# Performance work log

Hardware: AMD Instinct MI355X
Metric: run time of the kernel (lower is better)

The kernel has to match this reference:

```python
import jax, jax.numpy as jnp
import numpy as np
from jax import lax

B, C, H, W = 32, 684, 16, 64
HID, A, CK, K = 256, 512, 512, 11


def setup_inputs() -> dict:
    key = jax.random.key(0)
    ks = jax.random.split(key, 12)
    s = 0.02
    return {
        "cnn_features": jax.random.normal(ks[0], (B, C, H, W), jnp.float32),
        "hidden": jax.random.normal(ks[1], (B, HID), jnp.float32),
        "alpha_sum": jax.random.uniform(ks[2], (B, 1, H, W), jnp.float32),
        "image_mask": jnp.ones((B, 1, H, W), jnp.float32),
        # hidden_weight: Linear(HID -> A)
        "Wh": jax.random.normal(ks[3], (A, HID), jnp.float32) * s,
        "bh": jnp.zeros((A,), jnp.float32),
        # encoder_feature_conv: Conv2d(C -> A, 1x1) == pointwise linear
        "Wec": jax.random.normal(ks[4], (A, C), jnp.float32) * s,
        "bec": jnp.zeros((A,), jnp.float32),
        # attention_conv: Conv2d(1 -> CK, 11x11, pad 5, no bias)
        "Wac": jax.random.normal(ks[5], (CK, 1, K, K), jnp.float32) * s,
        # attention_weight: Linear(CK -> A, no bias)
        "Waw": jax.random.normal(ks[6], (A, CK), jnp.float32) * s,
        # alpha_convert: Linear(A -> 1)
        "Wv": jax.random.normal(ks[7], (1, A), jnp.float32) * s,
        "bv": jnp.zeros((1,), jnp.float32),
    }


def reference(cnn_features, hidden, alpha_sum, image_mask,
              Wh, bh, Wec, bec, Wac, Waw, Wv, bv):
    # query = hidden_weight(hidden): [B, A]
    query = hidden @ Wh.T + bh
    # attention_conv(alpha_sum): [B, CK, H, W]
    ast = lax.conv_general_dilated(
        alpha_sum, Wac, window_strides=(1, 1),
        padding=[(K // 2, K // 2), (K // 2, K // 2)],
        dimension_numbers=("NCHW", "OIHW", "NCHW"))
    # attention_weight on permuted conv output: [B, H, W, A]
    coverage_alpha = jnp.einsum("bkhw,ak->bhwa", ast, Waw)
    # encoder_feature_conv (1x1 conv == pointwise linear): [B, H, W, A]
    cnn_trans = jnp.einsum("bchw,ac->bhwa", cnn_features, Wec) + bec
    # additive attention score
    alpha_score = jnp.tanh(query[:, None, None, :] + coverage_alpha + cnn_trans)
    # alpha_convert -> scalar energy per position: [B, H, W]
    energy = jnp.einsum("bhwa,a->bhw", alpha_score, Wv[0]) + bv[0]
    energy = energy - energy.max()  # global max-subtract as in original
    energy_exp = jnp.exp(energy) * image_mask[:, 0]
    denom = energy_exp.sum(axis=(-1, -2))[:, None, None] + 1e-10
    alpha = energy_exp / denom  # [B, H, W]
    alpha_sum_new = alpha[:, None, :, :] + alpha_sum  # [B, 1, H, W]
    # context: weighted spatial sum over features -> [B, C]
    context_vector = jnp.einsum("bhw,bchw->bc", alpha, cnn_features)
    return (context_vector, alpha, alpha_sum_new)
```

## Files before the change

### kernel.cpp

```cpp
#include <hip/hip_runtime.h>
#include <math.h>

#define Bn   32
#define Cn   684
#define Hn   16
#define Wn   64
#define HWn  1024
#define HIDn 256
#define An   512
#define KKn  121
#define CREAL 805
#define CPAD 832
#define NSTEP 26

#define OUT_ALPHA 21888
#define OUT_ASUM  (21888 + 32768)

typedef short short8 __attribute__((ext_vector_type(8)));
typedef float floatx4 __attribute__((ext_vector_type(4)));

__device__ __forceinline__ unsigned short f2bf(float f) {
    union { float f; unsigned int i; } v; v.f = f;
    unsigned int i = v.i;
    return (unsigned short)((i + 0x7fffu + ((i >> 16) & 1u)) >> 16);
}
__device__ __forceinline__ unsigned int pack2bf(float v0, float v1) {
    unsigned int u0 = __float_as_uint(v0), u1 = __float_as_uint(v1);
    u0 = (u0 + 0x7fffu + ((u0 >> 16) & 1u)) >> 16;
    u1 = (u1 + 0x7fffu + ((u1 >> 16) & 1u)) & 0xffff0000u;
    return u0 | u1;
}

__global__ __launch_bounds__(256) void k_prep(
    const float* __restrict__ hidden,
    const float* __restrict__ Wh,
    const float* __restrict__ bh,
    const float* __restrict__ bec,
    const float* __restrict__ Wec,
    const float* __restrict__ Wac,
    const float* __restrict__ Waw,
    float* __restrict__ query,
    unsigned short* __restrict__ VTbf)
{
    __shared__ float sbuf[512];
    const int blk = blockIdx.x, t = threadIdx.x;
    if (blk < 512) {
        const int a = blk;
        sbuf[t]       = Waw[(size_t)a * 512 + t];
        sbuf[t + 256] = Waw[(size_t)a * 512 + t + 256];
        __syncthreads();
        for (int cp = t; cp < Cn; cp += 256)
            VTbf[(size_t)a * CPAD + cp] = f2bf(Wec[(size_t)a * Cn + cp]);
        if (t < KKn) {
            float s = 0.f;
            #pragma unroll 8
            for (int k = 0; k < 512; ++k)
                s = fmaf(sbuf[k], Wac[k * KKn + t], s);
            VTbf[(size_t)a * CPAD + Cn + t] = f2bf(s);
        }
        for (int cp = CREAL + t; cp < CPAD; cp += 256)
            VTbf[(size_t)a * CPAD + cp] = 0;
    } else {
        const int b = blk - 512;
        sbuf[t] = (t < HIDn) ? hidden[b * HIDn + t] : 0.f;
        __syncthreads();
        for (int a = t; a < An; a += 256) {
            const float4* wp = (const float4*)(Wh + (size_t)a * HIDn);
            float s = bh[a] + bec[a];
            #pragma unroll 8
            for (int i = 0; i < HIDn / 4; ++i) {
                float4 w = wp[i];
                s = fmaf(sbuf[4 * i],     w.x, s);
                s = fmaf(sbuf[4 * i + 1], w.y, s);
                s = fmaf(sbuf[4 * i + 2], w.z, s);
                s = fmaf(sbuf[4 * i + 3], w.w, s);
            }
            query[b * An + a] = s;
        }
    }
}

__global__ __launch_bounds__(256, 2) void k_energy(
    const float* __restrict__ X,
    const float* __restrict__ asum,
    const float* __restrict__ Wv,
    const float* __restrict__ query,
    const unsigned short* __restrict__ VTbf,
    float* __restrict__ energy)
{
    __shared__ float plane[11 * 74 + 2];
    __shared__ float qs[512];
    __shared__ float wvs[512];
    __shared__ float red[64 * 65];

    const int t = threadIdx.x;
    const int hh = blockIdx.x, b = blockIdx.y;
    const int w = t >> 6, lane = t & 63;
    const int q = lane >> 4, r = lane & 15;

    for (int i = t; i < 11 * 74; i += 256) {
        int di = i / 74, cc = i - di * 74;
        int h2 = hh + di - 5, w2 = cc - 5;
        float v = 0.f;
        if (h2 >= 0 && h2 < Hn && w2 >= 0 && w2 < Wn)
            v = asum[b * HWn + h2 * Wn + w2];
        plane[i] = v;
    }
    qs[t]        = query[b * An + t];
    qs[t + 256]  = query[b * An + t + 256];
    wvs[t]       = Wv[t];
    wvs[t + 256] = Wv[t + 256];
    __syncthreads();

    floatx4 acc[4][8];
    #pragma unroll
    for (int mf = 0; mf < 4; ++mf)
        #pragma unroll
        for (int nf = 0; nf < 8; ++nf)
            acc[mf][nf] = (floatx4){0.f, 0.f, 0.f, 0.f};

    const float* Xb = X + (size_t)b * Cn * HWn + hh * Wn;
    const unsigned short* Bb = VTbf + (size_t)(w * 128) * CPAD;

    for (int ch = 0; ch < 21; ++ch) {
        const int c0 = ch * 32;
        short8 bfr[8];
        #pragma unroll
        for (int nf = 0; nf < 8; ++nf)
            bfr[nf] = *(const short8*)(Bb + (size_t)(nf * 16 + r) * CPAD + c0 + q * 8);
        short8 af[4];
        #pragma unroll
        for (int mf = 0; mf < 4; ++mf) {
            const int m = mf * 16 + r;
            const float* xp = Xb + (size_t)(c0 + q * 8) * HWn + m;
            unsigned int pk[4];
            #pragma unroll
            for (int jj = 0; jj < 4; ++jj)
                pk[jj] = pack2bf(xp[(size_t)(2 * jj) * HWn], xp[(size_t)(2 * jj + 1) * HWn]);
            union { unsigned int u[4]; short8 s; } cv;
            cv.u[0] = pk[0]; cv.u[1] = pk[1]; cv.u[2] = pk[2]; cv.u[3] = pk[3];
            af[mf] = cv.s;
        }
        #pragma unroll
        for (int mf = 0; mf < 4; ++mf)
            #pragma unroll
            for (int nf = 0; nf < 8; ++nf)
                acc[mf][nf] = __builtin_amdgcn_mfma_f32_16x16x32_bf16(
                    af[mf], bfr[nf], acc[mf][nf], 0, 0, 0);
    }
    for (int ch = 21; ch < NSTEP; ++ch) {
        const int c0 = ch * 32;
        short8 bfr[8];
        #pragma unroll
        for (int nf = 0; nf < 8; ++nf)
            bfr[nf] = *(const short8*)(Bb + (size_t)(nf * 16 + r) * CPAD + c0 + q * 8);
        short8 af[4];
        #pragma unroll
        for (int mf = 0; mf < 4; ++mf) {
            const int m = mf * 16 + r;
            float v[8];
            #pragma unroll
            for (int jj = 0; jj < 8; ++jj) {
                int row = c0 + q * 8 + jj;
                float x;
                if (row < Cn) {
                    x = Xb[(size_t)row * HWn + m];
                } else if (row < CREAL) {
                    int ij = row - Cn; int di = ij / 11, dj = ij - di * 11;
                    x = plane[di * 74 + m + dj];
                } else {
                    x = 0.f;
                }
                v[jj] = x;
            }
            union { unsigned int u[4]; short8 s; } cv;
            #pragma unroll
            for (int jj = 0; jj < 4; ++jj)
                cv.u[jj] = pack2bf(v[2 * jj], v[2 * jj + 1]);
            af[mf] = cv.s;
        }
        #pragma unroll
        for (int mf = 0; mf < 4; ++mf)
            #pragma unroll
            for (int nf = 0; nf < 8; ++nf)
                acc[mf][nf] = __builtin_amdgcn_mfma_f32_16x16x32_bf16(
                    af[mf], bfr[nf], acc[mf][nf], 0, 0, 0);
    }

    float ep[16];
    #pragma unroll
    for (int i = 0; i < 16; ++i) ep[i] = 0.f;
    #pragma unroll
    for (int nf = 0; nf < 8; ++nf) {
        int n = w * 128 + nf * 16 + r;
        float qv = qs[n], wv = wvs[n];
        #pragma unroll
        for (int mf = 0; mf < 4; ++mf)
            #pragma unroll
            for (int rg = 0; rg < 4; ++rg) {
                float x = acc[mf][nf][rg] + qv;
                float e2 = __expf(2.f * x);
                float th = 1.f - 2.f * __builtin_amdgcn_rcpf(e2 + 1.f);
                ep[mf * 4 + rg] += wv * th;
            }
    }
    __syncthreads();
    #pragma unroll
    for (int mf = 0; mf < 4; ++mf)
        #pragma unroll
        for (int rg = 0; rg < 4; ++rg)
            red[(mf * 16 + q * 4 + rg) * 65 + w * 16 + r] = ep[mf * 4 + rg];
    __syncthreads();
    if (t < 64) {
        float s = 0.f;
        #pragma unroll 16
        for (int i = 0; i < 64; ++i) s += red[t * 65 + i];
        energy[b * HWn + hh * Wn + t] = s;
    }
}

__global__ __launch_bounds__(1024) void k_softmax(
    const float* __restrict__ energy,
    const float* __restrict__ mask, const float* __restrict__ asum,
    float* __restrict__ alpha_f, float* __restrict__ out)
{
    __shared__ float sm[16];
    __shared__ float bc[2];
    const int b = blockIdx.x, t = threadIdx.x;
    float e = energy[b * HWn + t];
    float m = e;
    for (int off = 32; off >= 1; off >>= 1) m = fmaxf(m, __shfl_down(m, off, 64));
    if ((t & 63) == 0) sm[t >> 6] = m;
    __syncthreads();
    if (t == 0) {
        float mm = sm[0];
        for (int i = 1; i < 16; ++i) mm = fmaxf(mm, sm[i]);
        bc[0] = mm;
    }
    __syncthreads();
    float ex = expf(e - bc[0]) * mask[b * HWn + t];
    float s = ex;
    for (int off = 32; off >= 1; off >>= 1) s += __shfl_down(s, off, 64);
    __syncthreads();
    if ((t & 63) == 0) sm[t >> 6] = s;
    __syncthreads();
    if (t == 0) {
        float tot = 0.f;
        for (int i = 0; i < 16; ++i) tot += sm[i];
        bc[1] = tot + 1e-10f;
    }
    __syncthreads();
    float alpha = ex / bc[1];
    alpha_f[b * HWn + t] = alpha;
    out[OUT_ALPHA + b * HWn + t] = alpha;
    out[OUT_ASUM  + b * HWn + t] = alpha + asum[b * HWn + t];
}

__global__ __launch_bounds__(256) void k_context(
    const float* __restrict__ X, const float* __restrict__ alpha_f,
    float* __restrict__ out)
{
    const int t = threadIdx.x, lane = t & 63, wid = t >> 6;
    const int b = blockIdx.y;
    const int c = blockIdx.x * 4 + wid;
    const float* xp = X + ((size_t)(b * Cn + c)) * HWn;
    const float* ap = alpha_f + b * HWn;
    float s = 0.f;
    #pragma unroll
    for (int i = 0; i < 4; ++i) {
        int off = i * 256 + lane * 4;
        float4 x = *(const float4*)(xp + off);
        float4 a = *(const float4*)(ap + off);
        s = fmaf(a.x, x.x, s);
        s = fmaf(a.y, x.y, s);
        s = fmaf(a.z, x.z, s);
        s = fmaf(a.w, x.w, s);
    }
    for (int off = 32; off >= 1; off >>= 1) s += __shfl_down(s, off, 64);
    if (lane == 0) out[b * Cn + c] = s;
}

extern "C" void kernel_launch(void* const* d_in, const int* in_sizes, int n_in,
                              void* d_out, int out_size, void* d_ws, size_t ws_size,
                              hipStream_t stream)
{
    const float* X      = (const float*)d_in[0];
    const float* hidden = (const float*)d_in[1];
    const float* asum   = (const float*)d_in[2];
    const float* mask   = (const float*)d_in[3];
    const float* Wh     = (const float*)d_in[4];
    const float* bh     = (const float*)d_in[5];
    const float* Wec    = (const float*)d_in[6];
    const float* bec    = (const float*)d_in[7];
    const float* Wac    = (const float*)d_in[8];
    const float* Waw    = (const float*)d_in[9];
    const float* Wv     = (const float*)d_in[10];
    (void)in_sizes; (void)n_in; (void)out_size; (void)ws_size;

    float* out = (float*)d_out;
    float* ws = (float*)d_ws;
    float* query   = ws;
    float* energy  = ws + 16384;
    float* alpha_f = ws + 16384 + 32768;
    unsigned short* VTbf = (unsigned short*)(ws + 81920);

    k_prep    <<<dim3(544),     dim3(256),  0, stream>>>(hidden, Wh, bh, bec,
                                                         Wec, Wac, Waw, query, VTbf);
    k_energy  <<<dim3(16, 32),  dim3(256),  0, stream>>>(X, asum, Wv, query, VTbf, energy);
    k_softmax <<<dim3(32),      dim3(1024), 0, stream>>>(energy, mask, asum, alpha_f, out);
    k_context <<<dim3(171, 32), dim3(256),  0, stream>>>(X, alpha_f, out);
}
```

Before: 270.9 us.

## Double-buffer energy GEMM tiles in LDS, split N across blocks, fuse softmax into context

```diff
diff --git a/kernel.cpp b/kernel.cpp
--- a/kernel.cpp
+++ b/kernel.cpp
@@ -12,6 +12,7 @@
 #define CREAL 805
 #define CPAD 832
 #define NSTEP 26
+#define NBLK 256
 
 #define OUT_ALPHA 21888
 #define OUT_ASUM  (21888 + 32768)
@@ -29,6 +30,11 @@
     u0 = (u0 + 0x7fffu + ((u0 >> 16) & 1u)) >> 16;
     u1 = (u1 + 0x7fffu + ((u1 >> 16) & 1u)) & 0xffff0000u;
     return u0 | u1;
+}
+__device__ __forceinline__ void async_lds16(void* lds, const void* g) {
+    __builtin_amdgcn_global_load_lds(
+        (const __attribute__((address_space(1))) unsigned int*)g,
+        (__attribute__((address_space(3))) unsigned int*)lds, 16, 0, 0);
 }
 
 __global__ __launch_bounds__(256) void k_prep(
@@ -80,7 +86,18 @@
     }
 }
 
-__global__ __launch_bounds__(256, 2) void k_energy(
+__device__ __forceinline__ float fetchU(const float* __restrict__ X,
+                                        const float* plane,
+                                        int m, int row) {
+    if (row < Cn)   return X[(size_t)row * HWn + m];
+    if (row < CREAL) {
+        int ij = row - Cn; int di = ij / 11, dj = ij - di * 11;
+        return plane[di * 74 + m + dj];
+    }
+    return 0.f;
+}
+
+__global__ __launch_bounds__(256, 3) void k_energy(
     const float* __restrict__ X,
     const float* __restrict__ asum,
     const float* __restrict__ Wv,
@@ -88,15 +105,21 @@
     const unsigned short* __restrict__ VTbf,
     float* __restrict__ energy)
 {
+    __shared__ unsigned short As[2 * 64 * 40];
+    __shared__ unsigned short Bs[2 * 256 * 32];
     __shared__ float plane[11 * 74 + 2];
-    __shared__ float qs[512];
-    __shared__ float wvs[512];
-    __shared__ float red[64 * 65];
+    __shared__ float qs[NBLK];
+    __shared__ float wvs[NBLK];
 
     const int t = threadIdx.x;
-    const int hh = blockIdx.x, b = blockIdx.y;
+    const int nh = blockIdx.x, hh = blockIdx.y, b = blockIdx.z;
     const int w = t >> 6, lane = t & 63;
     const int q = lane >> 4, r = lane & 15;
+    const int nbase = nh * NBLK;
+    const int mA = t & 63;
+    const int koA = t >> 6;
+
+    const float* Xb = X + (size_t)b * Cn * HWn + hh * Wn;
 
     for (int i = t; i < 11 * 74; i += 256) {
         int di = i / 74, cc = i - di * 74;
@@ -106,94 +129,92 @@
             v = asum[b * HWn + h2 * Wn + w2];
         plane[i] = v;
     }
-    qs[t]        = query[b * An + t];
-    qs[t + 256]  = query[b * An + t + 256];
-    wvs[t]       = Wv[t];
-    wvs[t + 256] = Wv[t + 256];
-    __syncthreads();
-
-    floatx4 acc[4][8];
+    qs[t]  = query[b * An + nbase + t];
+    wvs[t] = Wv[nbase + t];
+    {
+        const float* xp = Xb + (size_t)(koA * 8) * HWn + mA;
+        unsigned int pk[4];
+        #pragma unroll
+        for (int jj = 0; jj < 4; ++jj)
+            pk[jj] = pack2bf(xp[(size_t)(2 * jj) * HWn], xp[(size_t)(2 * jj + 1) * HWn]);
+        *(uint4*)&As[mA * 40 + koA * 8] = make_uint4(pk[0], pk[1], pk[2], pk[3]);
+    }
+    #pragma unroll
+    for (int ii = 0; ii < 4; ++ii) {
+        int n0 = w * 64 + ii * 16;
+        int row = nbase + n0 + (lane >> 2);
+        int gc = (lane & 3) ^ ((lane >> 2) & 3);
+        async_lds16(&Bs[n0 * 32], VTbf + (size_t)row * CPAD + gc * 8);
+    }
+    __syncthreads();
+
+    floatx4 acc[4][4];
     #pragma unroll
     for (int mf = 0; mf < 4; ++mf)
         #pragma unroll
-        for (int nf = 0; nf < 8; ++nf)
+        for (int nf = 0; nf < 4; ++nf)
             acc[mf][nf] = (floatx4){0.f, 0.f, 0.f, 0.f};
 
-    const float* Xb = X + (size_t)b * Cn * HWn + hh * Wn;
-    const unsigned short* Bb = VTbf + (size_t)(w * 128) * CPAD;
-
-    for (int ch = 0; ch < 21; ++ch) {
-        const int c0 = ch * 32;
-        short8 bfr[8];
-        #pragma unroll
-        for (int nf = 0; nf < 8; ++nf)
-            bfr[nf] = *(const short8*)(Bb + (size_t)(nf * 16 + r) * CPAD + c0 + q * 8);
-        short8 af[4];
-        #pragma unroll
-        for (int mf = 0; mf < 4; ++mf) {
-            const int m = mf * 16 + r;
-            const float* xp = Xb + (size_t)(c0 + q * 8) * HWn + m;
+    for (int ch = 0; ch < NSTEP; ++ch) {
+        const int cur = ch & 1;
+        const unsigned short* Ab = As + cur * (64 * 40);
+        const unsigned short* Bb = Bs + cur * (256 * 32);
+
+        short8 af[4], bfr[4];
+        #pragma unroll
+        for (int mf = 0; mf < 4; ++mf)
+            af[mf] = *(const short8*)&Ab[(mf * 16 + r) * 40 + q * 8];
+        #pragma unroll
+        for (int nf = 0; nf < 4; ++nf)
+            bfr[nf] = *(const short8*)&Bb[(w * 64 + nf * 16 + r) * 32 + (q ^ (r & 3)) * 8];
+
+        if (ch < NSTEP - 1) {
+            const int c1 = (ch + 1) * 32;
+            unsigned short* Bn_ = Bs + (cur ^ 1) * (256 * 32);
+            #pragma unroll
+            for (int ii = 0; ii < 4; ++ii) {
+                int n0 = w * 64 + ii * 16;
+                int row = nbase + n0 + (lane >> 2);
+                int gc = (lane & 3) ^ ((lane >> 2) & 3);
+                async_lds16(&Bn_[n0 * 32], VTbf + (size_t)row * CPAD + c1 + gc * 8);
+            }
             unsigned int pk[4];
-            #pragma unroll
-            for (int jj = 0; jj < 4; ++jj)
-                pk[jj] = pack2bf(xp[(size_t)(2 * jj) * HWn], xp[(size_t)(2 * jj + 1) * HWn]);
-            union { unsigned int u[4]; short8 s; } cv;
-            cv.u[0] = pk[0]; cv.u[1] = pk[1]; cv.u[2] = pk[2]; cv.u[3] = pk[3];
-            af[mf] = cv.s;
+            if (c1 + 31 < Cn) {
+                const float* xp = Xb + (size_t)(c1 + koA * 8) * HWn + mA;
+                #pragma unroll
+                for (int jj = 0; jj < 4; ++jj)
+                    pk[jj] = pack2bf(xp[(size_t)(2 * jj) * HWn],
+                                     xp[(size_t)(2 * jj + 1) * HWn]);
+            } else {
+                float v[8];
+                #pragma unroll
+                for (int jj = 0; jj < 8; ++jj)
+                    v[jj] = fetchU(Xb, plane, mA, c1 + koA * 8 + jj);
+                #pragma unroll
+                for (int jj = 0; jj < 4; ++jj)
+                    pk[jj] = pack2bf(v[2 * jj], v[2 * jj + 1]);
+            }
+            *(uint4*)&As[(cur ^ 1) * (64 * 40) + mA * 40 + koA * 8] =
+                make_uint4(pk[0], pk[1], pk[2], pk[3]);
         }
+
         #pragma unroll
         for (int mf = 0; mf < 4; ++mf)
             #pragma unroll
-            for (int nf = 0; nf < 8; ++nf)
+            for (int nf = 0; nf < 4; ++nf)
                 acc[mf][nf] = __builtin_amdgcn_mfma_f32_16x16x32_bf16(
                     af[mf], bfr[nf], acc[mf][nf], 0, 0, 0);
-    }
-    for (int ch = 21; ch < NSTEP; ++ch) {
-        const int c0 = ch * 32;
-        short8 bfr[8];
-        #pragma unroll
-        for (int nf = 0; nf < 8; ++nf)
-            bfr[nf] = *(const short8*)(Bb + (size_t)(nf * 16 + r) * CPAD + c0 + q * 8);
-        short8 af[4];
-        #pragma unroll
-        for (int mf = 0; mf < 4; ++mf) {
-            const int m = mf * 16 + r;
-            float v[8];
-            #pragma unroll
-            for (int jj = 0; jj < 8; ++jj) {
-                int row = c0 + q * 8 + jj;
-                float x;
-                if (row < Cn) {
-                    x = Xb[(size_t)row * HWn + m];
-                } else if (row < CREAL) {
-                    int ij = row - Cn; int di = ij / 11, dj = ij - di * 11;
-                    x = plane[di * 74 + m + dj];
-                } else {
-                    x = 0.f;
-                }
-                v[jj] = x;
-            }
-            union { unsigned int u[4]; short8 s; } cv;
-            #pragma unroll
-            for (int jj = 0; jj < 4; ++jj)
-                cv.u[jj] = pack2bf(v[2 * jj], v[2 * jj + 1]);
-            af[mf] = cv.s;
-        }
-        #pragma unroll
-        for (int mf = 0; mf < 4; ++mf)
-            #pragma unroll
-            for (int nf = 0; nf < 8; ++nf)
-                acc[mf][nf] = __builtin_amdgcn_mfma_f32_16x16x32_bf16(
-                    af[mf], bfr[nf], acc[mf][nf], 0, 0, 0);
+
+        __syncthreads();
     }
 
     float ep[16];
     #pragma unroll
     for (int i = 0; i < 16; ++i) ep[i] = 0.f;
     #pragma unroll
-    for (int nf = 0; nf < 8; ++nf) {
-        int n = w * 128 + nf * 16 + r;
-        float qv = qs[n], wv = wvs[n];
+    for (int nf = 0; nf < 4; ++nf) {
+        int nl = w * 64 + nf * 16 + r;
+        float qv = qs[nl], wv = wvs[nl];
         #pragma unroll
         for (int mf = 0; mf < 4; ++mf)
             #pragma unroll
@@ -204,7 +225,7 @@
                 ep[mf * 4 + rg] += wv * th;
             }
     }
-    __syncthreads();
+    float* red = (float*)Bs;
     #pragma unroll
     for (int mf = 0; mf < 4; ++mf)
         #pragma unroll
@@ -215,69 +236,75 @@
         float s = 0.f;
         #pragma unroll 16
         for (int i = 0; i < 64; ++i) s += red[t * 65 + i];
-        energy[b * HWn + hh * Wn + t] = s;
-    }
-}
-
-__global__ __launch_bounds__(1024) void k_softmax(
+        atomicAdd(&energy[b * HWn + hh * Wn + t], s);
+    }
+}
+
+__global__ __launch_bounds__(256) void k_ctx(
+    const float* __restrict__ X,
     const float* __restrict__ energy,
-    const float* __restrict__ mask, const float* __restrict__ asum,
-    float* __restrict__ alpha_f, float* __restrict__ out)
-{
-    __shared__ float sm[16];
-    __shared__ float bc[2];
-    const int b = blockIdx.x, t = threadIdx.x;
-    float e = energy[b * HWn + t];
-    float m = e;
-    for (int off = 32; off >= 1; off >>= 1) m = fmaxf(m, __shfl_down(m, off, 64));
-    if ((t & 63) == 0) sm[t >> 6] = m;
-    __syncthreads();
-    if (t == 0) {
-        float mm = sm[0];
-        for (int i = 1; i < 16; ++i) mm = fmaxf(mm, sm[i]);
-        bc[0] = mm;
-    }
-    __syncthreads();
-    float ex = expf(e - bc[0]) * mask[b * HWn + t];
-    float s = ex;
-    for (int off = 32; off >= 1; off >>= 1) s += __shfl_down(s, off, 64);
-    __syncthreads();
-    if ((t & 63) == 0) sm[t >> 6] = s;
-    __syncthreads();
-    if (t == 0) {
-        float tot = 0.f;
-        for (int i = 0; i < 16; ++i) tot += sm[i];
-        bc[1] = tot + 1e-10f;
-    }
-    __syncthreads();
-    float alpha = ex / bc[1];
-    alpha_f[b * HWn + t] = alpha;
-    out[OUT_ALPHA + b * HWn + t] = alpha;
-    out[OUT_ASUM  + b * HWn + t] = alpha + asum[b * HWn + t];
-}
-
-__global__ __launch_bounds__(256) void k_context(
-    const float* __restrict__ X, const float* __restrict__ alpha_f,
+    const float* __restrict__ mask,
+    const float* __restrict__ asum,
     float* __restrict__ out)
 {
+    __shared__ float al[1024];
+    __shared__ float rsm[8];
+    const int bx = blockIdx.x, b = blockIdx.y;
     const int t = threadIdx.x, lane = t & 63, wid = t >> 6;
-    const int b = blockIdx.y;
-    const int c = blockIdx.x * 4 + wid;
+
+    float e[4], ex[4];
+    #pragma unroll
+    for (int i = 0; i < 4; ++i) e[i] = energy[b * HWn + i * 256 + t];
+    float m = fmaxf(fmaxf(e[0], e[1]), fmaxf(e[2], e[3]));
+    for (int off = 32; off >= 1; off >>= 1) m = fmaxf(m, __shfl_down(m, off, 64));
+    if (lane == 0) rsm[wid] = m;
+    __syncthreads();
+    if (t == 0)
+        rsm[4] = fmaxf(fmaxf(rsm[0], rsm[1]), fmaxf(rsm[2], rsm[3]));
+    __syncthreads();
+    const float M = rsm[4];
+    float s = 0.f;
+    #pragma unroll
+    for (int i = 0; i < 4; ++i) {
+        ex[i] = expf(e[i] - M) * mask[b * HWn + i * 256 + t];
+        s += ex[i];
+    }
+    for (int off = 32; off >= 1; off >>= 1) s += __shfl_down(s, off, 64);
+    __syncthreads();
+    if (lane == 0) rsm[wid] = s;
+    __syncthreads();
+    if (t == 0) rsm[5] = rsm[0] + rsm[1] + rsm[2] + rsm[3] + 1e-10f;
+    __syncthreads();
+    const float denom = rsm[5];
+    #pragma unroll
+    for (int i = 0; i < 4; ++i) al[i * 256 + t] = ex[i] / denom;
+    __syncthreads();
+
+    const int c = bx * 4 + wid;
     const float* xp = X + ((size_t)(b * Cn + c)) * HWn;
-    const float* ap = alpha_f + b * HWn;
-    float s = 0.f;
+    float s2 = 0.f;
     #pragma unroll
     for (int i = 0; i < 4; ++i) {
         int off = i * 256 + lane * 4;
         float4 x = *(const float4*)(xp + off);
-        float4 a = *(const float4*)(ap + off);
-        s = fmaf(a.x, x.x, s);
-        s = fmaf(a.y, x.y, s);
-        s = fmaf(a.z, x.z, s);
-        s = fmaf(a.w, x.w, s);
-    }
-    for (int off = 32; off >= 1; off >>= 1) s += __shfl_down(s, off, 64);
-    if (lane == 0) out[b * Cn + c] = s;
+        float4 a = *(const float4*)(al + off);
+        s2 = fmaf(a.x, x.x, s2);
+        s2 = fmaf(a.y, x.y, s2);
+        s2 = fmaf(a.z, x.z, s2);
+        s2 = fmaf(a.w, x.w, s2);
+    }
+    for (int off = 32; off >= 1; off >>= 1) s2 += __shfl_down(s2, off, 64);
+    if (lane == 0) out[b * Cn + c] = s2;
+
+    if (bx == 0) {
+        #pragma unroll
+        for (int i = 0; i < 4; ++i) {
+            int p = i * 256 + t;
+            float a = al[p];
+            out[OUT_ALPHA + b * HWn + p] = a;
+            out[OUT_ASUM  + b * HWn + p] = a + asum[b * HWn + p];
+        }
+    }
 }
 
 extern "C" void kernel_launch(void* const* d_in, const int* in_sizes, int n_in,
@@ -299,14 +326,13 @@
 
     float* out = (float*)d_out;
     float* ws = (float*)d_ws;
-    float* query   = ws;
-    float* energy  = ws + 16384;
-    float* alpha_f = ws + 16384 + 32768;
-    unsigned short* VTbf = (unsigned short*)(ws + 81920);
-
-    k_prep    <<<dim3(544),     dim3(256),  0, stream>>>(hidden, Wh, bh, bec,
-                                                         Wec, Wac, Waw, query, VTbf);
-    k_energy  <<<dim3(16, 32),  dim3(256),  0, stream>>>(X, asum, Wv, query, VTbf, energy);
-    k_softmax <<<dim3(32),      dim3(1024), 0, stream>>>(energy, mask, asum, alpha_f, out);
-    k_context <<<dim3(171, 32), dim3(256),  0, stream>>>(X, alpha_f, out);
-}
+    float* query  = ws;
+    float* energy = ws + 16384;
+    unsigned short* VTbf = (unsigned short*)(ws + 16384 + 32768);
+
+    hipMemsetAsync(energy, 0, HWn * Bn * sizeof(float), stream);
+    k_prep   <<<dim3(544),      dim3(256), 0, stream>>>(hidden, Wh, bh, bec,
+                                                        Wec, Wac, Waw, query, VTbf);
+    k_energy <<<dim3(2, 16, 32), dim3(256), 0, stream>>>(X, asum, Wv, query, VTbf, energy);
+    k_ctx    <<<dim3(171, 32),  dim3(256), 0, stream>>>(X, energy, mask, asum, out);
+}
```

Result: faster. 252.9 us (-6.7%).
